# Optimization experiments

Hardware: AMD Instinct MI355X
Metric: run time of the kernel (lower is better)

Reference implementation:

```python
import jax, jax.numpy as jnp
import numpy as np

N, P, C, K = 16, 2048, 64, 16
EPS = 1e-5


def _bn(x, gamma, beta, axes):
    # training-mode batchnorm: biased variance over all dims except channel (last)
    m = jnp.mean(x, axis=axes, keepdims=True)
    v = jnp.var(x, axis=axes, keepdims=True)
    return (x - m) * jax.lax.rsqrt(v + EPS) * gamma + beta


def setup_inputs() -> dict:
    key = jax.random.key(0)
    ks = jax.random.split(key, 16)
    w = lambda k, shape: jax.random.normal(k, shape, jnp.float32) * 0.05
    inp = {"features": jax.random.normal(ks[0], (N, C, P), jnp.float32)}
    # edge-conv MLP: layer 0 takes 2*C input channels
    inp["w0"], inp["b0"] = w(ks[1], (C, 2 * C)), jnp.zeros((C,), jnp.float32)
    inp["g0"], inp["be0"] = jnp.ones((C,), jnp.float32), jnp.zeros((C,), jnp.float32)
    inp["w1"], inp["b1"] = w(ks[2], (C, C)), jnp.zeros((C,), jnp.float32)
    inp["g1"], inp["be1"] = jnp.ones((C,), jnp.float32), jnp.zeros((C,), jnp.float32)
    inp["w2"], inp["b2"] = w(ks[3], (C, C)), jnp.zeros((C,), jnp.float32)
    inp["g2"], inp["be2"] = jnp.ones((C,), jnp.float32), jnp.zeros((C,), jnp.float32)
    # shortcut 1x1 conv + BN
    inp["ws"], inp["bs"] = w(ks[4], (C, C)), jnp.zeros((C,), jnp.float32)
    inp["gs"], inp["bes"] = jnp.ones((C,), jnp.float32), jnp.zeros((C,), jnp.float32)
    return inp


def reference(features, w0, b0, g0, be0, w1, b1, g1, be1, w2, b2, g2, be2, ws, bs, gs, bes):
    # index != 0: features come in as (N, C, P) -> (N, P, C)
    X = jnp.transpose(features, (0, 2, 1))  # (N, P, C)

    # --- KNN via full pairwise squared distances ---
    r = jnp.sum(X * X, axis=-1)  # (N, P)
    d = r[:, :, None] - 2.0 * jnp.einsum('npc,nqc->npq', X, X) + r[:, None, :]
    _, idx = jax.lax.top_k(-d, K + 1)
    idx = idx[:, :, 1:]  # drop self, (N, P, K)

    # --- irregular gather + edge-feature concat ---
    f = X[jnp.arange(X.shape[0])[:, None, None], idx]  # (N, P, K, C)
    fc = jnp.broadcast_to(X[:, :, None, :], f.shape)   # center feature tiled
    h = jnp.concatenate([fc, fc - f], axis=-1)         # (N, P, K, 2C)

    def conv_bn_relu(h, w, b, g, be):
        h = jnp.einsum('npki,oi->npko', h, w) + b
        return jax.nn.relu(_bn(h, g, be, (0, 1, 2)))

    h = conv_bn_relu(h, w0, b0, g0, be0)
    h = conv_bn_relu(h, w1, b1, g1, be1)
    h = conv_bn_relu(h, w2, b2, g2, be2)
    h = jnp.mean(h, axis=2)  # aggregate over K -> (N, P, C)

    # shortcut: 1x1 conv + BN on center features
    sc = jnp.einsum('npi,oi->npo', X, ws) + bs
    sc = _bn(sc, gs, bes, (0, 1))

    out = jax.nn.relu(h + sc)           # (N, P, C)
    return jnp.transpose(out, (0, 2, 1))  # (N, C, P) to match torch layout
```

## Files before the change

### kernel.cpp

```cpp
#include <hip/hip_runtime.h>

using u16    = unsigned short;
using u32    = unsigned int;
using u64    = unsigned long long;
using bf16x8 = __attribute__((ext_vector_type(8))) short;
using f32x4  = __attribute__((ext_vector_type(4))) float;
using u16x4  = __attribute__((ext_vector_type(4))) u16;

#define NB   16
#define PP   2048
#define CC   64
#define KK   16
#define MROWS (NB*PP*KK)
#define NPTS  (NB*PP)

__device__ __forceinline__ float b2f(u16 u) { return __uint_as_float(((unsigned)u) << 16); }
__device__ __forceinline__ u16 f2b(float f) {
  unsigned u = __float_as_uint(f);
  return (u16)((u + 0x7fffu + ((u >> 16) & 1u)) >> 16);
}

__device__ __forceinline__ u64 dkey(float d, int qi) {
  unsigned u = __float_as_uint(d);
  u = u ^ (((unsigned)((int)u >> 31)) | 0x80000000u);
  return ((u64)u << 32) | (unsigned)qi;
}

template<bool UP>
__device__ __forceinline__ void ce(u64 &a, u64 &b) {
  const bool lt = a < b;
  const u64 lo = lt ? a : b;
  const u64 hi = lt ? b : a;
  if (UP) { a = lo; b = hi; } else { a = hi; b = lo; }
}

__device__ __forceinline__ void sort16(u64 (&v)[16]) {
  #pragma unroll
  for (int k = 2; k <= 16; k <<= 1) {
    #pragma unroll
    for (int j = k >> 1; j > 0; j >>= 1) {
      #pragma unroll
      for (int i = 0; i < 16; ++i) {
        const int l = i ^ j;
        if (l > i) {
          if ((i & k) == 0) ce<true>(v[i], v[l]);
          else              ce<false>(v[i], v[l]);
        }
      }
    }
  }
}

__device__ __forceinline__ void merge16(u64 (&dl)[16], const u64 (&nb)[16]) {
  u64 t[16];
  #pragma unroll
  for (int s = 0; s < 16; ++s) {
    const u64 a = dl[s], b = nb[15 - s];
    t[s] = a < b ? a : b;
  }
  #pragma unroll
  for (int j = 8; j > 0; j >>= 1) {
    #pragma unroll
    for (int i = 0; i < 16; ++i) {
      const int l = i ^ j;
      if (l > i) ce<true>(t[i], t[l]);
    }
  }
  #pragma unroll
  for (int s = 0; s < 16; ++s) dl[s] = t[s];
}

__global__ __launch_bounds__(256) void prep_k(const float* __restrict__ F,
                                              u16* __restrict__ Xb,
                                              u16* __restrict__ X3,
                                              float* __restrict__ r) {
  int gidx = blockIdx.x * 256 + threadIdx.x;
  int n = gidx >> 11, p = gidx & 2047;
  const float* src = F + (size_t)n * CC * PP + p;
  float rr = 0.f;
  u16 ha[CC], ma[CC], la[CC];
  #pragma unroll
  for (int c = 0; c < CC; ++c) {
    const float x = src[(size_t)c * PP];
    rr += x * x;
    const u16 h = f2b(x);
    const float eh = x - b2f(h);
    const u16 m = f2b(eh);
    const float el = eh - b2f(m);
    const u16 lo_ = f2b(el);
    ha[c] = h; ma[c] = m; la[c] = lo_;
  }
  u16* db = Xb + (size_t)gidx * CC;
  u16* d3 = X3 + (size_t)gidx * 128;
  #pragma unroll
  for (int c = 0; c < CC; c += 8) {
    bf16x8 wh, wm, wl;
    #pragma unroll
    for (int j = 0; j < 8; ++j) { wh[j] = (short)ha[c+j]; wm[j] = (short)ma[c+j]; wl[j] = (short)la[c+j]; }
    *(bf16x8*)(db + c)      = wh;
    *(bf16x8*)(d3 + c)      = wm;
    *(bf16x8*)(d3 + 64 + c) = wl;
  }
  r[gidx] = rr;
}

__global__ __launch_bounds__(256) void cvtw_k(const float* __restrict__ w0, const float* __restrict__ w1,
                                              const float* __restrict__ w2, const float* __restrict__ wsb,
                                              u16* __restrict__ b0, u16* __restrict__ b1,
                                              u16* __restrict__ b2, u16* __restrict__ bs) {
  int i = blockIdx.x * 256 + threadIdx.x;
  if (i < 8192)        b0[i]          = f2b(w0[i]);
  else if (i < 12288)  b1[i - 8192]   = f2b(w1[i - 8192]);
  else if (i < 16384)  b2[i - 12288]  = f2b(w2[i - 12288]);
  else if (i < 20480)  bs[i - 16384]  = f2b(wsb[i - 16384]);
}

__global__ __launch_bounds__(512) __attribute__((amdgpu_waves_per_eu(4)))
void knn_k(const u16* __restrict__ Xb, const u16* __restrict__ X3,
           const float* __restrict__ r, u64* __restrict__ part) {
  extern __shared__ char ldsraw[];
  u16*   XpL = (u16*)ldsraw;
  u16*   XqL = (u16*)(ldsraw + 25600);
  float* D   = (float*)(ldsraw + 25600);
  u64*   mb  = (u64*)ldsraw;

  const int n  = blockIdx.x >> 7;
  const int pb = ((blockIdx.x >> 2) & 31) * 64;
  const int qq = blockIdx.x & 3;
  const int qstart = qq * 512;
  const int t  = threadIdx.x;
  const int l  = t & 63, w = t >> 6;
  const int P = w & 3, qhalf = w >> 2;
  const int lo = l & 15, hi4 = l >> 4;

  const u16*  Xbn = Xb + (size_t)(n * PP) * CC;
  const u16*  X3n = X3 + (size_t)(n * PP) * 128;
  const float* rb = r + n * PP;

  {
    {
      const int row = t >> 3, unit = t & 7;
      *(bf16x8*)(XpL + row * 200 + unit * 8) =
        *(const bf16x8*)(Xbn + (size_t)(pb + row) * CC + unit * 8);
    }
    #pragma unroll
    for (int k = 0; k < 2; ++k) {
      const int u = t + k * 512;
      const int row = u >> 4, unit = u & 15;
      *(bf16x8*)(XpL + row * 200 + 64 + unit * 8) =
        *(const bf16x8*)(X3n + (size_t)(pb + row) * 128 + unit * 8);
    }
  }

  u64 dl[16];
  #pragma unroll
  for (int s = 0; s < 16; ++s) dl[s] = ~0ULL;

  #pragma unroll 1
  for (int qb = qstart; qb < qstart + 512; qb += 128) {
    __syncthreads();
    {
      #pragma unroll
      for (int k = 0; k < 2; ++k) {
        const int u = t + k * 512;
        const int row = u >> 3, unit = u & 7;
        *(bf16x8*)(XqL + row * 200 + unit * 8) =
          *(const bf16x8*)(Xbn + (size_t)(qb + row) * CC + unit * 8);
      }
      #pragma unroll
      for (int k = 0; k < 4; ++k) {
        const int u = t + k * 512;
        const int row = u >> 4, unit = u & 15;
        *(bf16x8*)(XqL + row * 200 + 64 + unit * 8) =
          *(const bf16x8*)(X3n + (size_t)(qb + row) * 128 + unit * 8);
      }
    }
    __syncthreads();

    bf16x8 ah[2], am[2], al[2];
    #pragma unroll
    for (int kb = 0; kb < 2; ++kb) {
      const int base = (P * 16 + lo) * 200 + kb * 32 + hi4 * 8;
      ah[kb] = *(const bf16x8*)(XpL + base);
      am[kb] = *(const bf16x8*)(XpL + base + 64);
      al[kb] = *(const bf16x8*)(XpL + base + 128);
    }

    f32x4 acc[4];
    #pragma unroll
    for (int Q = 0; Q < 4; ++Q) { f32x4 z = {0.f, 0.f, 0.f, 0.f}; acc[Q] = z; }

    #pragma unroll
    for (int Q = 0; Q < 4; ++Q) {
      const int qrow = qhalf * 64 + Q * 16 + lo;
      #pragma unroll
      for (int kb = 0; kb < 2; ++kb) {
        const int base = qrow * 200 + kb * 32 + hi4 * 8;
        const bf16x8 bh = *(const bf16x8*)(XqL + base);
        const bf16x8 bm = *(const bf16x8*)(XqL + base + 64);
        const bf16x8 bl = *(const bf16x8*)(XqL + base + 128);
        acc[Q] = __builtin_amdgcn_mfma_f32_16x16x32_bf16(ah[kb], bh, acc[Q], 0, 0, 0);
        acc[Q] = __builtin_amdgcn_mfma_f32_16x16x32_bf16(am[kb], bh, acc[Q], 0, 0, 0);
        acc[Q] = __builtin_amdgcn_mfma_f32_16x16x32_bf16(ah[kb], bm, acc[Q], 0, 0, 0);
        acc[Q] = __builtin_amdgcn_mfma_f32_16x16x32_bf16(al[kb], bh, acc[Q], 0, 0, 0);
        acc[Q] = __builtin_amdgcn_mfma_f32_16x16x32_bf16(ah[kb], bl, acc[Q], 0, 0, 0);
        acc[Q] = __builtin_amdgcn_mfma_f32_16x16x32_bf16(am[kb], bm, acc[Q], 0, 0, 0);
      }
    }
    __syncthreads();

    {
      #pragma unroll
      for (int Q = 0; Q < 4; ++Q) {
        const int qloc  = qhalf * 64 + Q * 16 + lo;
        const int qglob = qb + qloc;
        const float rq  = rb[qglob];
        const int bidx = qloc >> 2, qrem = qloc & 3;
        #pragma unroll
        for (int e = 0; e < 4; ++e) {
          const int p = P * 16 + hi4 * 4 + e;
          float d = rq - 2.f * acc[Q][e];
          if (qglob == pb + p) d = 3.0e38f;
          const int swz = ((bidx ^ ((p & 7) << 2)) << 2) + qrem;
          D[p * 132 + swz] = d;
        }
      }
    }
    __syncthreads();

    {
      u64 nb[16];
      const int prow = l;
      const float* drow = D + (size_t)prow * 132;
      const int u4 = (prow & 7) * 4;
      #pragma unroll
      for (int bb = 0; bb < 4; ++bb) {
        const int b = w * 4 + bb;
        const float4 dv = *(const float4*)(drow + ((b ^ u4) * 4));
        const int qg = qb + b * 4;
        nb[bb*4+0] = dkey(dv.x, qg+0);
        nb[bb*4+1] = dkey(dv.y, qg+1);
        nb[bb*4+2] = dkey(dv.z, qg+2);
        nb[bb*4+3] = dkey(dv.w, qg+3);
      }
      sort16(nb);
      merge16(dl, nb);
    }
  }

  __syncthreads();
  {
    if (t >= 256) {
      #pragma unroll
      for (int s = 0; s < 16; ++s) mb[s * 256 + (t - 256)] = dl[s];
    }
    __syncthreads();
    if (t < 256) {
      u64 nb[16];
      #pragma unroll
      for (int s = 0; s < 16; ++s) nb[s] = mb[s * 256 + t];
      merge16(dl, nb);
    }
    __syncthreads();
    if (t < 256) {
      #pragma unroll
      for (int s = 0; s < 16; ++s) mb[s * 256 + t] = dl[s];
    }
    __syncthreads();
    if (t < 64) {
      #pragma unroll 1
      for (int j = 1; j < 4; ++j) {
        u64 nb[16];
        #pragma unroll
        for (int s = 0; s < 16; ++s) nb[s] = mb[s * 256 + (t + 64 * j)];
        merge16(dl, nb);
      }
      u64* outp = part + (((size_t)n * PP + pb + t) * 4 + qq) * 16;
      #pragma unroll
      for (int s = 0; s < 16; ++s) outp[s] = dl[s];
    }
  }
}

__global__ __launch_bounds__(256) void knnm_k(const u64* __restrict__ part,
                                              int* __restrict__ idx) {
  const int row = blockIdx.x * 256 + threadIdx.x;
  const u64* p = part + (size_t)row * 64;
  u64 dl[16];
  #pragma unroll
  for (int s = 0; s < 16; ++s) dl[s] = p[s];
  #pragma unroll 1
  for (int j = 1; j < 4; ++j) {
    u64 nb[16];
    #pragma unroll
    for (int s = 0; s < 16; ++s) nb[s] = p[j * 16 + s];
    merge16(dl, nb);
  }
  #pragma unroll
  for (int s = 0; s < 16; ++s)
    idx[(size_t)row * KK + s] = (int)(dl[s] & 0xFFFFFFFFu);
}

template<int KIN, bool GATHER, bool BNRELU>
__global__ __launch_bounds__(256) void conv_k(const u16* __restrict__ in,
                                              const int* __restrict__ idxp,
                                              const u16* __restrict__ wb,
                                              const float* __restrict__ bias,
                                              const float* __restrict__ st,
                                              u16* __restrict__ yout,
                                              float* __restrict__ partials) {
  constexpr int NKB = KIN / 32;
  __shared__ float sred[4][4][32];
  const int t = threadIdx.x;
  const int wv = t >> 6, l = t & 63, hi = l >> 4, lo = l & 15;
  const int rbase = blockIdx.x * 256 + wv * 64;

  bf16x8 wf[4][NKB];
  #pragma unroll
  for (int ob = 0; ob < 4; ++ob)
    #pragma unroll
    for (int kb = 0; kb < NKB; ++kb)
      wf[ob][kb] = *(const bf16x8*)(wb + (size_t)(ob*16 + lo) * KIN + kb*32 + hi*8);

  int qv[4];
  if constexpr (GATHER) {
    #pragma unroll
    for (int rb = 0; rb < 4; ++rb) {
      const int g = (rbase + rb*16) >> 4;
      qv[rb] = idxp[g * KK + lo];
    }
  }

  f32x4 acc[4][4];
  #pragma unroll
  for (int a = 0; a < 4; ++a)
    #pragma unroll
    for (int b = 0; b < 4; ++b) { f32x4 z = {0.f, 0.f, 0.f, 0.f}; acc[a][b] = z; }

  #pragma unroll
  for (int kb = 0; kb < NKB; ++kb) {
    float sv[8], tv[8];
    if constexpr (BNRELU) {
      const int k0 = kb*32 + hi*8;
      *(float4*)&sv[0] = *(const float4*)(st + k0);
      *(float4*)&sv[4] = *(const float4*)(st + k0 + 4);
      *(float4*)&tv[0] = *(const float4*)(st + KIN + k0);
      *(float4*)&tv[4] = *(const float4*)(st + KIN + k0 + 4);
    }
    bf16x8 af[4];
    #pragma unroll
    for (int rb = 0; rb < 4; ++rb) {
      if constexpr (GATHER) {
        const int g  = (rbase + rb*16) >> 4;
        const int k0 = kb*32 + hi*8;
        const bf16x8 fc = *(const bf16x8*)(in + (size_t)g * CC + (k0 & 63));
        if (kb < 2) {
          af[rb] = fc;
        } else {
          const int nn = g >> 11;
          const bf16x8 fv = *(const bf16x8*)(in + (size_t)(nn * PP + qv[rb]) * CC + (k0 & 63));
          bf16x8 df;
          #pragma unroll
          for (int j = 0; j < 8; ++j)
            df[j] = (short)f2b(b2f((u16)fc[j]) - b2f((u16)fv[j]));
          af[rb] = df;
        }
      } else {
        const int row = rbase + rb*16 + lo;
        const bf16x8 rv = *(const bf16x8*)(in + (size_t)row * KIN + kb*32 + hi*8);
        if constexpr (BNRELU) {
          bf16x8 tr;
          #pragma unroll
          for (int j = 0; j < 8; ++j) {
            const float x = fmaxf(b2f((u16)rv[j]) * sv[j] + tv[j], 0.f);
            tr[j] = (short)f2b(x);
          }
          af[rb] = tr;
        } else {
          af[rb] = rv;
        }
      }
    }
    #pragma unroll
    for (int ob = 0; ob < 4; ++ob)
      #pragma unroll
      for (int rb = 0; rb < 4; ++rb)
        acc[rb][ob] = __builtin_amdgcn_mfma_f32_16x16x32_bf16(wf[ob][kb], af[rb], acc[rb][ob], 0, 0, 0);
  }

  float ssum[16], qsum[16];
  #pragma unroll
  for (int j = 0; j < 16; ++j) { ssum[j] = 0.f; qsum[j] = 0.f; }
  #pragma unroll
  for (int ob = 0; ob < 4; ++ob) {
    const int o0 = ob*16 + hi*4;
    const float4 bv = *(const float4*)(bias + o0);
    #pragma unroll
    for (int rb = 0; rb < 4; ++rb) {
      const int row = rbase + rb*16 + lo;
      const float v0 = acc[rb][ob][0] + bv.x;
      const float v1 = acc[rb][ob][1] + bv.y;
      const float v2 = acc[rb][ob][2] + bv.z;
      const float v3 = acc[rb][ob][3] + bv.w;
      u16x4 pk; pk[0] = f2b(v0); pk[1] = f2b(v1); pk[2] = f2b(v2); pk[3] = f2b(v3);
      *(u16x4*)(yout + (size_t)row * CC + o0) = pk;
      ssum[ob*4+0] += v0; qsum[ob*4+0] += v0*v0;
      ssum[ob*4+1] += v1; qsum[ob*4+1] += v1*v1;
      ssum[ob*4+2] += v2; qsum[ob*4+2] += v2*v2;
      ssum[ob*4+3] += v3; qsum[ob*4+3] += v3*v3;
    }
  }
  #pragma unroll
  for (int m = 1; m < 16; m <<= 1) {
    #pragma unroll
    for (int j = 0; j < 16; ++j) {
      ssum[j] += __shfl_xor(ssum[j], m, 64);
      qsum[j] += __shfl_xor(qsum[j], m, 64);
    }
  }
  if (lo == 0) {
    #pragma unroll
    for (int j = 0; j < 16; ++j) {
      sred[wv][hi][j*2]   = ssum[j];
      sred[wv][hi][j*2+1] = qsum[j];
    }
  }
  __syncthreads();
  if (t < 128) {
    const int c = t & 63, half = t >> 6;
    const int slot = ((c >> 4) * 4 + (c & 3)) * 2 + half;
    const int h2 = (c >> 2) & 3;
    const float v = sred[0][h2][slot] + sred[1][h2][slot] + sred[2][h2][slot] + sred[3][h2][slot];
    partials[(size_t)blockIdx.x * 128 + half * 64 + c] = v;
  }
}

__global__ __launch_bounds__(256) void red1_k(const float* __restrict__ partials,
                                              float* __restrict__ out, int nwg) {
  __shared__ float accs[2][128];
  const int t = threadIdx.x, e = t & 127, h = t >> 7;
  float s = 0.f;
  for (int w = blockIdx.x + h * 64; w < nwg; w += 128)
    s += partials[(size_t)w * 128 + e];
  accs[h][e] = s;
  __syncthreads();
  if (t < 128) out[(size_t)blockIdx.x * 128 + t] = accs[0][t] + accs[1][t];
}

__global__ __launch_bounds__(128) void red2_k(const float* __restrict__ p2,
                                              const float* __restrict__ g,
                                              const float* __restrict__ be,
                                              float* __restrict__ st, float invM) {
  __shared__ float sq[128];
  const int t = threadIdx.x;
  float s = 0.f;
  #pragma unroll 8
  for (int w = 0; w < 64; ++w) s += p2[w * 128 + t];
  sq[t] = s;
  __syncthreads();
  if (t < 64) {
    const float S = sq[t], Q = sq[64 + t];
    const float m = S * invM;
    const float v = fmaxf(Q * invM - m * m, 0.f);
    const float sc = g[t] * rsqrtf(v + 1e-5f);
    st[t] = sc;
    st[64 + t] = be[t] - m * sc;
  }
}

__global__ __launch_bounds__(256) void final_k(const u16* __restrict__ y2,
                                               const u16* __restrict__ ysc,
                                               const float* __restrict__ st2,
                                               const float* __restrict__ stS,
                                               float* __restrict__ out) {
  __shared__ float ot[64][68];
  const int b = blockIdx.x, t = threadIdx.x;
  const int n = b >> 5, p0 = (b & 31) * 64;
  const int phh = t >> 2, jh = t & 3, c0 = jh * 16;
  const int g = n * PP + p0 + phh;
  float acc[16];
  #pragma unroll
  for (int i = 0; i < 16; ++i) acc[i] = 0.f;
  float sv[16], tv[16];
  #pragma unroll
  for (int i = 0; i < 16; ++i) { sv[i] = st2[c0 + i]; tv[i] = st2[64 + c0 + i]; }
  for (int k = 0; k < KK; ++k) {
    const u16* rp = y2 + ((size_t)g * KK + k) * CC + c0;
    const bf16x8 v0 = *(const bf16x8*)rp;
    const bf16x8 v1 = *(const bf16x8*)(rp + 8);
    #pragma unroll
    for (int j = 0; j < 8; ++j) {
      acc[j]     += fmaxf(b2f((u16)v0[j]) * sv[j]     + tv[j],     0.f);
      acc[8 + j] += fmaxf(b2f((u16)v1[j]) * sv[8 + j] + tv[8 + j], 0.f);
    }
  }
  const u16* sp = ysc + (size_t)g * CC + c0;
  const bf16x8 s0 = *(const bf16x8*)sp;
  const bf16x8 s1 = *(const bf16x8*)(sp + 8);
  #pragma unroll
  for (int i = 0; i < 16; ++i) {
    const float scx = b2f((u16)(i < 8 ? s0[i] : s1[i - 8])) * stS[c0 + i] + stS[64 + c0 + i];
    ot[c0 + i][phh] = fmaxf(acc[i] * (1.f / 16.f) + scx, 0.f);
  }
  __syncthreads();
  const int c = t >> 2, pc = t & 3;
  const float* src = &ot[c][pc * 16];
  float* dst = out + (size_t)n * CC * PP + (size_t)c * PP + p0 + pc * 16;
  #pragma unroll
  for (int j = 0; j < 16; j += 4) *(float4*)(dst + j) = *(const float4*)(src + j);
}

extern "C" void kernel_launch(void* const* d_in, const int* in_sizes, int n_in,
                              void* d_out, int out_size, void* d_ws, size_t ws_size,
                              hipStream_t stream) {
  (void)in_sizes; (void)n_in; (void)out_size; (void)ws_size;
  const float* F   = (const float*)d_in[0];
  const float* w0  = (const float*)d_in[1];
  const float* b0  = (const float*)d_in[2];
  const float* g0  = (const float*)d_in[3];
  const float* be0 = (const float*)d_in[4];
  const float* w1  = (const float*)d_in[5];
  const float* b1  = (const float*)d_in[6];
  const float* g1  = (const float*)d_in[7];
  const float* be1 = (const float*)d_in[8];
  const float* w2  = (const float*)d_in[9];
  const float* b2  = (const float*)d_in[10];
  const float* g2  = (const float*)d_in[11];
  const float* be2 = (const float*)d_in[12];
  const float* wS  = (const float*)d_in[13];
  const float* bS  = (const float*)d_in[14];
  const float* gS  = (const float*)d_in[15];
  const float* beS = (const float*)d_in[16];

  char* ws = (char*)d_ws;
  size_t off = 0;
  auto carve = [&](size_t bytes) -> void* {
    void* p = ws + off;
    off += (bytes + 255) & ~(size_t)255;
    return p;
  };
  u16*   Xb       = (u16*)  carve((size_t)NPTS * CC * 2);
  u16*   X3       = (u16*)  carve((size_t)NPTS * 128 * 2);
  float* rr       = (float*)carve((size_t)NPTS * 4);
  int*   idx      = (int*)  carve((size_t)NPTS * KK * 4);
  u16*   wb0      = (u16*)  carve(8192 * 2);
  u16*   wb1      = (u16*)  carve(4096 * 2);
  u16*   wb2      = (u16*)  carve(4096 * 2);
  u16*   wbs      = (u16*)  carve(4096 * 2);
  u16*   y        = (u16*)  carve((size_t)MROWS * CC * 2);
  u16*   ysc      = (u16*)  carve((size_t)NPTS * CC * 2);
  float* partials = (float*)carve((size_t)2048 * 128 * 4);
  float* p2       = (float*)carve((size_t)64 * 128 * 4);
  float* st0      = (float*)carve(128 * 4);
  float* st1      = (float*)carve(128 * 4);
  float* st2      = (float*)carve(128 * 4);
  float* stS      = (float*)carve(128 * 4);

  u64* part = (u64*)y;

  prep_k<<<NPTS / 256, 256, 0, stream>>>(F, Xb, X3, rr);
  cvtw_k<<<80, 256, 0, stream>>>(w0, w1, w2, wS, wb0, wb1, wb2, wbs);
  knn_k<<<NB * 32 * 4, 512, 76800, stream>>>(Xb, X3, rr, part);
  knnm_k<<<NPTS / 256, 256, 0, stream>>>(part, idx);

  conv_k<128, true,  false><<<MROWS / 256, 256, 0, stream>>>(Xb, idx, wb0, b0, nullptr, y, partials);
  red1_k<<<64, 256, 0, stream>>>(partials, p2, MROWS / 256);
  red2_k<<<1, 128, 0, stream>>>(p2, g0, be0, st0, 1.f / (float)MROWS);

  conv_k<64, false, true><<<MROWS / 256, 256, 0, stream>>>(y, nullptr, wb1, b1, st0, y, partials);
  red1_k<<<64, 256, 0, stream>>>(partials, p2, MROWS / 256);
  red2_k<<<1, 128, 0, stream>>>(p2, g1, be1, st1, 1.f / (float)MROWS);

  conv_k<64, false, true><<<MROWS / 256, 256, 0, stream>>>(y, nullptr, wb2, b2, st1, y, partials);
  red1_k<<<64, 256, 0, stream>>>(partials, p2, MROWS / 256);
  red2_k<<<1, 128, 0, stream>>>(p2, g2, be2, st2, 1.f / (float)MROWS);

  conv_k<64, false, false><<<NPTS / 256, 256, 0, stream>>>(Xb, nullptr, wbs, bS, nullptr, ysc, partials);
  red1_k<<<64, 256, 0, stream>>>(partials, p2, NPTS / 256);
  red2_k<<<1, 128, 0, stream>>>(p2, gS, beS, stS, 1.f / (float)NPTS);

  final_k<<<NB * (PP / 64), 256, 0, stream>>>(y, ysc, st2, stS, (float*)d_out);
}
```

Before: 451.6 us.

## Restructure KNN kernel to 256 threads with register-resident point tiles

The KNN distance kernel now runs 256 threads instead of 512, and each wave handles 16 points against all 128 queries per tile (8 accumulators instead of 4). The point-tile operands are loaded once from global memory straight into registers instead of being staged in LDS, which cuts LDS use to a single 51 KB static buffer and should allow more blocks per CU. Each thread now sorts and merges two 16-candidate groups per tile, and the final in-block merge drops one level. In exchange each thread carries more registers (acc[8] plus the bf16x8 fragments) and does more serial sort work, which may lower occupancy or raise latency.

```diff
diff --git a/kernel.cpp b/kernel.cpp
--- a/kernel.cpp
+++ b/kernel.cpp
@@ -115,14 +115,12 @@
   else if (i < 20480)  bs[i - 16384]  = f2b(wsb[i - 16384]);
 }
 
-__global__ __launch_bounds__(512) __attribute__((amdgpu_waves_per_eu(4)))
+__global__ __launch_bounds__(256)
 void knn_k(const u16* __restrict__ Xb, const u16* __restrict__ X3,
            const float* __restrict__ r, u64* __restrict__ part) {
-  extern __shared__ char ldsraw[];
-  u16*   XpL = (u16*)ldsraw;
-  u16*   XqL = (u16*)(ldsraw + 25600);
-  float* D   = (float*)(ldsraw + 25600);
-  u64*   mb  = (u64*)ldsraw;
+  __shared__ u16 XqL[128 * 200];
+  float* D  = (float*)XqL;
+  u64*   mb = (u64*)XqL;
 
   const int n  = blockIdx.x >> 7;
   const int pb = ((blockIdx.x >> 2) & 31) * 64;
@@ -130,25 +128,23 @@
   const int qstart = qq * 512;
   const int t  = threadIdx.x;
   const int l  = t & 63, w = t >> 6;
-  const int P = w & 3, qhalf = w >> 2;
   const int lo = l & 15, hi4 = l >> 4;
+  const int prow = t & 63;
+  const int qh2  = t >> 6;
+  const int u4   = (prow & 7) * 4;
 
   const u16*  Xbn = Xb + (size_t)(n * PP) * CC;
   const u16*  X3n = X3 + (size_t)(n * PP) * 128;
   const float* rb = r + n * PP;
 
+  bf16x8 ah[2], am[2], al[2];
   {
-    {
-      const int row = t >> 3, unit = t & 7;
-      *(bf16x8*)(XpL + row * 200 + unit * 8) =
-        *(const bf16x8*)(Xbn + (size_t)(pb + row) * CC + unit * 8);
-    }
-    #pragma unroll
-    for (int k = 0; k < 2; ++k) {
-      const int u = t + k * 512;
-      const int row = u >> 4, unit = u & 15;
-      *(bf16x8*)(XpL + row * 200 + 64 + unit * 8) =
-        *(const bf16x8*)(X3n + (size_t)(pb + row) * 128 + unit * 8);
+    const size_t rowb = (size_t)(pb + w * 16 + lo);
+    #pragma unroll
+    for (int kb = 0; kb < 2; ++kb) {
+      ah[kb] = *(const bf16x8*)(Xbn + rowb * CC  + kb * 32 + hi4 * 8);
+      am[kb] = *(const bf16x8*)(X3n + rowb * 128 + kb * 32 + hi4 * 8);
+      al[kb] = *(const bf16x8*)(X3n + rowb * 128 + 64 + kb * 32 + hi4 * 8);
     }
   }
 
@@ -161,15 +157,15 @@
     __syncthreads();
     {
       #pragma unroll
-      for (int k = 0; k < 2; ++k) {
-        const int u = t + k * 512;
+      for (int k = 0; k < 4; ++k) {
+        const int u = t + k * 256;
         const int row = u >> 3, unit = u & 7;
         *(bf16x8*)(XqL + row * 200 + unit * 8) =
           *(const bf16x8*)(Xbn + (size_t)(qb + row) * CC + unit * 8);
       }
       #pragma unroll
-      for (int k = 0; k < 4; ++k) {
-        const int u = t + k * 512;
+      for (int k = 0; k < 8; ++k) {
+        const int u = t + k * 256;
         const int row = u >> 4, unit = u & 15;
         *(bf16x8*)(XqL + row * 200 + 64 + unit * 8) =
           *(const bf16x8*)(X3n + (size_t)(qb + row) * 128 + unit * 8);
@@ -177,22 +173,13 @@
     }
     __syncthreads();
 
-    bf16x8 ah[2], am[2], al[2];
-    #pragma unroll
-    for (int kb = 0; kb < 2; ++kb) {
-      const int base = (P * 16 + lo) * 200 + kb * 32 + hi4 * 8;
-      ah[kb] = *(const bf16x8*)(XpL + base);
-      am[kb] = *(const bf16x8*)(XpL + base + 64);
-      al[kb] = *(const bf16x8*)(XpL + base + 128);
-    }
-
-    f32x4 acc[4];
-    #pragma unroll
-    for (int Q = 0; Q < 4; ++Q) { f32x4 z = {0.f, 0.f, 0.f, 0.f}; acc[Q] = z; }
-
-    #pragma unroll
-    for (int Q = 0; Q < 4; ++Q) {
-      const int qrow = qhalf * 64 + Q * 16 + lo;
+    f32x4 acc[8];
+    #pragma unroll
+    for (int Q = 0; Q < 8; ++Q) { f32x4 z = {0.f, 0.f, 0.f, 0.f}; acc[Q] = z; }
+
+    #pragma unroll
+    for (int Q = 0; Q < 8; ++Q) {
+      const int qrow = Q * 16 + lo;
       #pragma unroll
       for (int kb = 0; kb < 2; ++kb) {
         const int base = qrow * 200 + kb * 32 + hi4 * 8;
@@ -211,14 +198,14 @@
 
     {
       #pragma unroll
-      for (int Q = 0; Q < 4; ++Q) {
-        const int qloc  = qhalf * 64 + Q * 16 + lo;
+      for (int Q = 0; Q < 8; ++Q) {
+        const int qloc  = Q * 16 + lo;
         const int qglob = qb + qloc;
         const float rq  = rb[qglob];
         const int bidx = qloc >> 2, qrem = qloc & 3;
         #pragma unroll
         for (int e = 0; e < 4; ++e) {
-          const int p = P * 16 + hi4 * 4 + e;
+          const int p = w * 16 + hi4 * 4 + e;
           float d = rq - 2.f * acc[Q][e];
           if (qglob == pb + p) d = 3.0e38f;
           const int swz = ((bidx ^ ((p & 7) << 2)) << 2) + qrem;
@@ -228,14 +215,13 @@
     }
     __syncthreads();
 
-    {
+    #pragma unroll
+    for (int half = 0; half < 2; ++half) {
       u64 nb[16];
-      const int prow = l;
       const float* drow = D + (size_t)prow * 132;
-      const int u4 = (prow & 7) * 4;
       #pragma unroll
       for (int bb = 0; bb < 4; ++bb) {
-        const int b = w * 4 + bb;
+        const int b = qh2 * 8 + half * 4 + bb;
         const float4 dv = *(const float4*)(drow + ((b ^ u4) * 4));
         const int qg = qb + b * 4;
         nb[bb*4+0] = dkey(dv.x, qg+0);
@@ -250,35 +236,21 @@
 
   __syncthreads();
   {
-    if (t >= 256) {
-      #pragma unroll
-      for (int s = 0; s < 16; ++s) mb[s * 256 + (t - 256)] = dl[s];
-    }
-    __syncthreads();
-    if (t < 256) {
+    #pragma unroll
+    for (int s = 0; s < 16; ++s) mb[s * 256 + t] = dl[s];
+  }
+  __syncthreads();
+  if (t < 64) {
+    #pragma unroll 1
+    for (int j = 1; j < 4; ++j) {
       u64 nb[16];
       #pragma unroll
-      for (int s = 0; s < 16; ++s) nb[s] = mb[s * 256 + t];
+      for (int s = 0; s < 16; ++s) nb[s] = mb[s * 256 + (t + 64 * j)];
       merge16(dl, nb);
     }
-    __syncthreads();
-    if (t < 256) {
-      #pragma unroll
-      for (int s = 0; s < 16; ++s) mb[s * 256 + t] = dl[s];
-    }
-    __syncthreads();
-    if (t < 64) {
-      #pragma unroll 1
-      for (int j = 1; j < 4; ++j) {
-        u64 nb[16];
-        #pragma unroll
-        for (int s = 0; s < 16; ++s) nb[s] = mb[s * 256 + (t + 64 * j)];
-        merge16(dl, nb);
-      }
-      u64* outp = part + (((size_t)n * PP + pb + t) * 4 + qq) * 16;
-      #pragma unroll
-      for (int s = 0; s < 16; ++s) outp[s] = dl[s];
-    }
+    u64* outp = part + (((size_t)n * PP + pb + t) * 4 + qq) * 16;
+    #pragma unroll
+    for (int s = 0; s < 16; ++s) outp[s] = dl[s];
   }
 }
 
@@ -560,7 +532,7 @@
 
   prep_k<<<NPTS / 256, 256, 0, stream>>>(F, Xb, X3, rr);
   cvtw_k<<<80, 256, 0, stream>>>(w0, w1, w2, wS, wb0, wb1, wb2, wbs);
-  knn_k<<<NB * 32 * 4, 512, 76800, stream>>>(Xb, X3, rr, part);
+  knn_k<<<NB * 32 * 4, 256, 0, stream>>>(Xb, X3, rr, part);
   knnm_k<<<NPTS / 256, 256, 0, stream>>>(part, idx);
 
   conv_k<128, true,  false><<<MROWS / 256, 256, 0, stream>>>(Xb, idx, wb0, b0, nullptr, y, partials);
```

Measured after the change: 390.0 us (median of 3 runs). -13.7%, faster.
